# Optimization experiments

Measured on AMD Instinct MI355X. Metric: run time of the kernel, lower is better.

The kernel has to match this reference:

```python
import jax, jax.numpy as jnp
import numpy as np


def _antideriv_tanh(t):
    # int tanh dx = |x| + log1p(exp(-2|x|))  (numerically stable)
    a = jnp.abs(t)
    return a + jnp.log1p(jnp.exp(-2.0 * a))


def _deriv_tanh(t):
    th = jnp.tanh(t)
    return 1.0 - th * th


def setup_inputs() -> dict:
    key = jax.random.key(0)
    ks = jax.random.split(key, 9)
    d, m, nTh, r, nex = 63, 256, 3, 10, 4096
    x = jax.random.normal(ks[0], (nex, d + 1), dtype=jnp.float32)
    W0 = jax.random.normal(ks[1], (m, d + 1), dtype=jnp.float32) / jnp.sqrt(float(d + 1))
    b0 = jax.random.normal(ks[2], (m,), dtype=jnp.float32) * 0.1
    Wd = jax.random.normal(ks[3], (nTh - 1, m, m), dtype=jnp.float32) / jnp.sqrt(float(m))
    bd = jax.random.normal(ks[4], (nTh - 1, m), dtype=jnp.float32) * 0.1
    wv = jax.random.normal(ks[5], (m,), dtype=jnp.float32)
    A = jax.random.normal(ks[6], (r, d + 1), dtype=jnp.float32) / jnp.sqrt(float(d + 1))
    cw = jax.random.normal(ks[7], (d + 1,), dtype=jnp.float32) * 0.1
    cb = jax.random.normal(ks[8], (), dtype=jnp.float32) * 0.1
    return {"x": x, "W0": W0, "b0": b0, "Wd": Wd, "bd": bd, "wv": wv, "A": A, "cw": cw, "cb": cb}


def reference(x, W0, b0, Wd, bd, wv, A, cw, cb):
    """Phi.trHess: returns (grad of Phi wrt x, trace of Hessian of Phi), shapes [nex, d+1], [nex]."""
    nTh = Wd.shape[0] + 1
    h = 1.0 / (nTh - 1)
    m = W0.shape[0]
    nex = x.shape[0]
    d = x.shape[1] - 1

    symA = A.T @ A                                  # [d+1, d+1]

    # ---- forward propagation of ResNN, keeping hidden states u and preactivations ----
    opening = x @ W0.T + b0                         # [nex, m]
    u = [_antideriv_tanh(opening)]
    pre = []                                        # preactivations of layers 1..nTh-1
    feat = u[0]
    for i in range(1, nTh):
        p = feat @ Wd[i - 1].T + bd[i - 1]          # [nex, m]
        pre.append(p)
        feat = feat + h * _antideriv_tanh(p)
        u.append(feat)

    tanhopen = jnp.tanh(opening)                    # [nex, m]

    # ---- backward z chain (Eq. 11): gradient of w'N(x) wrt x ----
    z = [None] * nTh
    for i in range(nTh - 1, 0, -1):
        term = wv[:, None] if i == nTh - 1 else z[i + 1]      # [m,1] or [m,nex]
        z[i] = term + h * (Wd[i - 1].T @ (jnp.tanh(pre[i - 1]).T * term))
    z0 = W0.T @ (tanhopen.T * z[1])                 # [d+1, nex]
    grad = z0 + symA @ x.T + cw[:, None]            # [d+1, nex]

    # ---- trace of Hessian (Eq. 13) ----
    Kopen = W0[:, :d]                               # [m, d]  (spatial part of opening weight)
    temp = _deriv_tanh(opening.T) * z[1]            # [m, nex]
    # sum_{m,d} temp[m,n] * Kopen[m,d]^2
    trH = jnp.einsum('mn,m->n', temp, jnp.sum(Kopen * Kopen, axis=1))

    Jac = Kopen[:, :, None] * tanhopen.T[:, None, :]          # [m, d, nex]
    for i in range(1, nTh):
        KJ = (Wd[i - 1] @ Jac.reshape(m, d * nex)).reshape(m, d, nex)
        term = wv[:, None] if i == nTh - 1 else z[i + 1]
        p = pre[i - 1].T                             # [m, nex]
        t_i = jnp.einsum('mn,mdn->n', _deriv_tanh(p) * term, KJ * KJ)
        trH = trH + h * t_i
        Jac = Jac + h * jnp.tanh(p)[:, None, :] * KJ

    trH = trH + jnp.trace(symA[:d, :d])
    return grad.T, trH
```

## Files before the change

kernel.cpp:

```cpp
#include <hip/hip_runtime.h>
#include <hip/hip_bf16.h>

#define NEX 4096
#define M   256
#define NM  (NEX*M)

typedef __attribute__((ext_vector_type(8))) short short8;
typedef __attribute__((ext_vector_type(16))) float floatx16;
typedef __attribute__((ext_vector_type(4))) unsigned short ushort4v;

__device__ inline unsigned short f2bfu(float x) {
    __hip_bfloat16 h = __float2bfloat16(x);
    union { __hip_bfloat16 b; unsigned short u; } cv; cv.b = h;
    return cv.u;
}
__device__ inline float bfu2f(unsigned short u) {
    union { unsigned short u; __hip_bfloat16 b; } cv; cv.u = u;
    return __bfloat162float(cv.b);
}

__global__ void k_prep(const float* __restrict__ Wd, const float* __restrict__ W0,
                       const float* __restrict__ A,
                       unsigned short* __restrict__ FB,
                       unsigned short* __restrict__ FBT,
                       unsigned short* __restrict__ FW0,
                       unsigned short* __restrict__ FWT,
                       unsigned short* __restrict__ FSA,
                       float* __restrict__ FA,
                       float* __restrict__ ksq, float* __restrict__ trace) {
    int b = blockIdx.x, t = threadIdx.x;
    int lane = t & 63, l31 = lane & 31, lhi = lane >> 5;
    if (b < 64) {
        int combo = b*4 + (t >> 6);
        int l = combo >> 7, rest = combo & 127;
        int mtile = rest >> 4, kstep = rest & 15;
        const float* src = Wd + l*65536 + (mtile*32 + l31)*256 + kstep*16 + lhi*8;
        int off = l*65536 + (mtile*16 + kstep)*512 + lane*8;
        #pragma unroll
        for (int e = 0; e < 8; ++e) FB[off+e] = f2bfu(src[e]);
    } else if (b < 128) {
        int combo = (b-64)*4 + (t >> 6);
        int l = combo >> 7, rest = combo & 127;
        int kt = rest >> 4, ms = rest & 15;
        const float* src = Wd + l*65536 + (ms*16 + lhi*8)*256 + kt*32 + l31;
        int off = l*65536 + (kt*16 + ms)*512 + lane*8;
        #pragma unroll
        for (int e = 0; e < 8; ++e) FBT[off+e] = f2bfu(src[e*256]);
    } else if (b < 136) {
        int combo = (b-128)*4 + (t >> 6);
        int mt = combo >> 2, ks = combo & 3;
        const float* src = W0 + (mt*32 + l31)*64 + ks*16 + lhi*8;
        int off = combo*512 + lane*8;
        #pragma unroll
        for (int e = 0; e < 8; ++e) FW0[off+e] = f2bfu(src[e]);
    } else if (b < 144) {
        int combo = (b-136)*4 + (t >> 6);
        int ct = combo >> 4, ms = combo & 15;
        const float* src = W0 + (ms*16 + lhi*8)*64 + ct*32 + l31;
        int off = combo*512 + lane*8;
        #pragma unroll
        for (int e = 0; e < 8; ++e) FWT[off+e] = f2bfu(src[e*64]);
    } else if (b < 146) {
        int combo = (b-144)*4 + (t >> 6);
        int ct = combo >> 2, ks = combo & 3;
        int c = ct*32 + l31;
        int off = combo*512 + lane*8;
        #pragma unroll
        for (int e = 0; e < 8; ++e) {
            int j = ks*16 + lhi*8 + e;
            float s = 0.f;
            #pragma unroll
            for (int r = 0; r < 10; ++r) s += A[r*64+c] * A[r*64+j];
            FSA[off+e] = f2bfu(s);
        }
    } else if (b == 146) {
        float s = 0.f;
        for (int dd = 0; dd < 63; dd++) { float v = W0[t*64+dd]; s += v*v; }
        ksq[t] = s;
        float p = 0.f;
        for (int idx = t; idx < 630; idx += 256) {
            int r = idx / 63, i = idx % 63;
            float v = A[r*64+i]; p += v*v;
        }
        for (int off = 32; off; off >>= 1) p += __shfl_down(p, off, 64);
        __shared__ float red[4];
        if ((t & 63) == 0) red[t >> 6] = p;
        __syncthreads();
        if (t == 0) trace[0] = red[0]+red[1]+red[2]+red[3];
    } else {
        int q = (b-147)*256 + t;
        int tl = q & 63, frag = q >> 6;
        int d  = (frag >> 4)*32 + (tl & 31);
        int m0 = (frag & 15)*16 + (tl >> 5)*8;
        float* dst = FA + q*8;
        #pragma unroll
        for (int e = 0; e < 8; ++e)
            dst[e] = (d == 63) ? 0.f : W0[(m0 + e)*64 + d];
    }
}

__global__ __launch_bounds__(512, 2) void k_fb(
        const float* __restrict__ x, const float* __restrict__ b0,
        const float* __restrict__ bd, const float* __restrict__ wv,
        const float* __restrict__ cw,
        const unsigned short* __restrict__ FW0,
        const unsigned short* __restrict__ FB,
        const unsigned short* __restrict__ FBT,
        const unsigned short* __restrict__ FWT,
        const unsigned short* __restrict__ FSA,
        float* __restrict__ tanhopen, float* __restrict__ tp0g,
        float* __restrict__ tp1g, float* __restrict__ z2T, float* __restrict__ z1T,
        float* __restrict__ out) {
    __shared__ __align__(16) unsigned short Buh[8192], Bul[8192];
    __shared__ __align__(16) unsigned short Bxh[2048], Bxl[2048];
    __shared__ __align__(16) float bounce[8224];
    __shared__ float b0s[256], bd0s[256], bd1s[256], wvs[256], cws[64];
    int n0 = blockIdx.x * 32, t = threadIdx.x;
    int lane = t & 63, w = t >> 6, l31 = lane & 31, lhi = lane >> 5;

    if (t < 256) { b0s[t]=b0[t]; bd0s[t]=bd[t]; bd1s[t]=bd[256+t]; wvs[t]=wv[t]; }
    if (t < 64) cws[t] = cw[t];
    if (t < 256) {
        int tl = t & 63;
        int ex = tl & 31, k0 = (t >> 6)*16 + (tl >> 5)*8;
        const float* xp = x + (n0+ex)*64 + k0;
        short8 h8, l8;
        #pragma unroll
        for (int e = 0; e < 8; ++e) {
            float v = xp[e];
            unsigned short h = f2bfu(v);
            h8[e] = (short)h; l8[e] = (short)f2bfu(v - bfu2f(h));
        }
        *reinterpret_cast<short8*>(&Bxh[t*8]) = h8;
        *reinterpret_cast<short8*>(&Bxl[t*8]) = l8;
    }
    __syncthreads();

#define MROW(r) (w*32 + ((r)&3) + 8*((r)>>2) + 4*lhi)

#define MFMA2(AH, BH, BL) do { \
    acc = __builtin_amdgcn_mfma_f32_32x32x16_bf16(AH, BH, acc, 0, 0, 0); \
    acc = __builtin_amdgcn_mfma_f32_32x32x16_bf16(AH, BL, acc, 0, 0, 0); \
} while (0)

#define GEMM256(PH) do { \
    for (int ks = 0; ks < 16; ++ks) { \
        short8 Ah = *reinterpret_cast<const short8*>(PH + (w*16+ks)*512 + lane*8); \
        short8 Bh = *reinterpret_cast<const short8*>(&Buh[(ks*64+lane)*8]); \
        short8 Bl = *reinterpret_cast<const short8*>(&Bul[(ks*64+lane)*8]); \
        MFMA2(Ah, Bh, Bl); \
    } \
} while (0)

#define EPILOGUE(SVAL, DST, BVAL) do { \
    __syncthreads(); \
    _Pragma("unroll") \
    for (int r = 0; r < 16; ++r) bounce[l31*257 + MROW(r)] = SVAL[r]; \
    _Pragma("unroll") \
    for (int g = 0; g < 4; ++g) { \
        int ks_ = w*2 + (g>>1); \
        int lp_ = (g&1)*32 + l31; \
        int base_ = (ks_*64 + lp_)*8 + 4*lhi; \
        ushort4v h4, l4; \
        _Pragma("unroll") \
        for (int q = 0; q < 4; ++q) { \
            float v_ = BVAL[g*4+q]; \
            unsigned short h_ = f2bfu(v_); \
            h4[q] = h_; l4[q] = f2bfu(v_ - bfu2f(h_)); \
        } \
        *reinterpret_cast<ushort4v*>(&Buh[base_]) = h4; \
        *reinterpret_cast<ushort4v*>(&Bul[base_]) = l4; \
    } \
    __syncthreads(); \
    _Pragma("unroll") \
    for (int i = 0; i < 16; ++i) { \
        int f = t + i*512; int ex_ = f >> 8, m_ = f & 255; \
        DST[(n0+ex_)*256 + m_] = bounce[ex_*257 + m_]; \
    } \
} while (0)

    floatx16 acc;
    float sv[16], u0v[16], tp0v[16], z2v[16], cf[16];

    #pragma unroll
    for (int r = 0; r < 16; ++r) acc[r] = 0.f;
    #pragma unroll
    for (int ks = 0; ks < 4; ++ks) {
        short8 Ah = *reinterpret_cast<const short8*>(FW0 + (w*4+ks)*512 + lane*8);
        short8 Bh = *reinterpret_cast<const short8*>(&Bxh[(ks*64+lane)*8]);
        short8 Bl = *reinterpret_cast<const short8*>(&Bxl[(ks*64+lane)*8]);
        MFMA2(Ah, Bh, Bl);
    }
    #pragma unroll
    for (int r = 0; r < 16; ++r) {
        float p = acc[r] + b0s[MROW(r)];
        float a = fabsf(p);
        float e = __expf(-2.f*a);
        float th = (1.f - e) * __builtin_amdgcn_rcpf(1.f + e);
        sv[r] = __builtin_copysignf(th, p);
        u0v[r] = a + __logf(1.f + e);
    }
    EPILOGUE(sv, tanhopen, u0v);

    #pragma unroll
    for (int r = 0; r < 16; ++r) acc[r] = 0.f;
    GEMM256(FB);
    #pragma unroll
    for (int r = 0; r < 16; ++r) {
        float p = acc[r] + bd0s[MROW(r)];
        float a = fabsf(p);
        float e = __expf(-2.f*a);
        float th = (1.f - e) * __builtin_amdgcn_rcpf(1.f + e);
        tp0v[r] = __builtin_copysignf(th, p);
        u0v[r] += 0.5f*(a + __logf(1.f + e));
    }
    EPILOGUE(tp0v, tp0g, u0v);

    #pragma unroll
    for (int r = 0; r < 16; ++r) acc[r] = 0.f;
    GEMM256(FB + 65536);
    #pragma unroll
    for (int r = 0; r < 16; ++r) {
        float p = acc[r] + bd1s[MROW(r)];
        float a = fabsf(p);
        float e = __expf(-2.f*a);
        float th = (1.f - e) * __builtin_amdgcn_rcpf(1.f + e);
        cf[r] = __builtin_copysignf(th, p);
        z2v[r] = cf[r] * wvs[MROW(r)];
    }
    EPILOGUE(cf, tp1g, z2v);

    #pragma unroll
    for (int r = 0; r < 16; ++r) acc[r] = 0.f;
    GEMM256(FBT + 65536);
    #pragma unroll
    for (int r = 0; r < 16; ++r) {
        z2v[r] = wvs[MROW(r)] + 0.5f*acc[r];
        cf[r] = tp0v[r] * z2v[r];
    }
    EPILOGUE(z2v, z2T, cf);

    #pragma unroll
    for (int r = 0; r < 16; ++r) acc[r] = 0.f;
    GEMM256(FBT);
    #pragma unroll
    for (int r = 0; r < 16; ++r) {
        z2v[r] += 0.5f*acc[r];
        cf[r] = sv[r] * z2v[r];
    }
    EPILOGUE(z2v, z1T, cf);

    {
        int ct = w >> 2, seg = w & 3;
        #pragma unroll
        for (int r = 0; r < 16; ++r) acc[r] = 0.f;
        #pragma unroll
        for (int k2 = 0; k2 < 4; ++k2) {
            int ms = seg*4 + k2;
            short8 Ah = *reinterpret_cast<const short8*>(FWT + (ct*16+ms)*512 + lane*8);
            short8 Bh = *reinterpret_cast<const short8*>(&Buh[(ms*64+lane)*8]);
            short8 Bl = *reinterpret_cast<const short8*>(&Bul[(ms*64+lane)*8]);
            MFMA2(Ah, Bh, Bl);
        }
        if (seg == 0) {
            #pragma unroll
            for (int ks = 0; ks < 4; ++ks) {
                short8 Ah = *reinterpret_cast<const short8*>(FSA + (ct*4+ks)*512 + lane*8);
                short8 Bh = *reinterpret_cast<const short8*>(&Bxh[(ks*64+lane)*8]);
                short8 Bl = *reinterpret_cast<const short8*>(&Bxl[(ks*64+lane)*8]);
                MFMA2(Ah, Bh, Bl);
            }
        }
        __syncthreads();
        float* gpart = bounce;
        #pragma unroll
        for (int r = 0; r < 16; ++r) gpart[w*1024 + (2*r+lhi)*32 + l31] = acc[r];
        __syncthreads();
        int o0 = t*4, ex = o0 >> 6, c0 = o0 & 63;
        float4 gv;
        #pragma unroll
        for (int jj = 0; jj < 4; ++jj) {
            int c = c0 + jj;
            int ctx = c >> 5, cr = c & 31;
            int lh = (cr >> 2) & 1;
            int rr = (cr & 3) | ((cr >> 3) << 2);
            float s = cws[c];
            #pragma unroll
            for (int sg = 0; sg < 4; ++sg)
                s += gpart[(ctx*4+sg)*1024 + (2*rr+lh)*32 + ex];
            gv[jj] = s;
        }
        *reinterpret_cast<float4*>(&out[(n0+ex)*64 + c0]) = gv;
    }
#undef MROW
#undef MFMA2
#undef GEMM256
#undef EPILOGUE
}

__global__ __launch_bounds__(256, 3) void k_heavy_mfma(
        const float* __restrict__ tanhopen, const float* __restrict__ tp0,
        const float* __restrict__ tp1, const float* __restrict__ z2T,
        const float* __restrict__ z1T, const float* __restrict__ wv,
        const float* __restrict__ FA, const unsigned short* __restrict__ FB,
        const float* __restrict__ ksq, const float* __restrict__ trace,
        float* __restrict__ outTrH) {
    __shared__ __align__(16) unsigned short Bf[16384];
    __shared__ float ss[256], tp0s[256], w1s[256], w2s[256];
    __shared__ float red[4];
    int n = blockIdx.x, t = threadIdx.x;
    int lane = t & 63, w = t >> 6, l31 = lane & 31, lhi = lane >> 5;

    float sv = tanhopen[n*256 + t];
    float a0 = tp0[n*256 + t];
    float a1 = tp1[n*256 + t];
    ss[t] = sv;
    tp0s[t] = a0;
    w1s[t] = (1.f - a0*a0) * z2T[n*256 + t];
    w2s[t] = (1.f - a1*a1) * wv[t];
    float tot = (1.f - sv*sv) * z1T[n*256 + t] * ksq[t];
    __syncthreads();

    #pragma unroll
    for (int i = 0; i < 8; ++i) {
        int q = t + i*256;
        int frag = q >> 6, tl = q & 63;
        int k0 = (frag & 15)*16 + (tl >> 5)*8;
        const float* fp = FA + q*8;
        short8 v8;
        #pragma unroll
        for (int e = 0; e < 8; ++e)
            v8[e] = (short)f2bfu(fp[e] * ss[k0 + e]);
        *reinterpret_cast<short8*>(&Bf[q*8]) = v8;
    }
    __syncthreads();

    floatx16 acc[2][2];
    int mt0 = w*2, mt1 = w*2 + 1;
    float wtot = 0.f;

    const unsigned short* pA0 = FB + mt0*16*512 + lane*8;
    const unsigned short* pA1 = FB + mt1*16*512 + lane*8;
    const unsigned short* qB0 = &Bf[lane*8];
    const unsigned short* qB1 = &Bf[(16*64 + lane)*8];

#define LD8(P, KS) (*reinterpret_cast<const short8*>((P) + (KS)*512))
#define MFMA4(A0_, A1_, B0_, B1_) do { \
    acc[0][0] = __builtin_amdgcn_mfma_f32_32x32x16_bf16(A0_, B0_, acc[0][0], 0, 0, 0); \
    acc[0][1] = __builtin_amdgcn_mfma_f32_32x32x16_bf16(A0_, B1_, acc[0][1], 0, 0, 0); \
    acc[1][0] = __builtin_amdgcn_mfma_f32_32x32x16_bf16(A1_, B0_, acc[1][0], 0, 0, 0); \
    acc[1][1] = __builtin_amdgcn_mfma_f32_32x32x16_bf16(A1_, B1_, acc[1][1], 0, 0, 0); \
} while (0)

    #pragma unroll
    for (int jm = 0; jm < 2; ++jm)
        #pragma unroll
        for (int dh = 0; dh < 2; ++dh)
            #pragma unroll
            for (int r = 0; r < 16; ++r) acc[jm][dh][r] = 0.f;

    {
        short8 A0s[4], A1s[4], B0s[2], B1s[2];
        A0s[0] = LD8(pA0, 0); A1s[0] = LD8(pA1, 0);
        A0s[1] = LD8(pA0, 1); A1s[1] = LD8(pA1, 1);
        A0s[2] = LD8(pA0, 2); A1s[2] = LD8(pA1, 2);
        B0s[0] = LD8(qB0, 0); B1s[0] = LD8(qB1, 0);
        #pragma unroll
        for (int ks = 0; ks < 16; ++ks) {
            if (ks + 3 < 16) {
                A0s[(ks+3)&3] = LD8(pA0, ks+3);
                A1s[(ks+3)&3] = LD8(pA1, ks+3);
            }
            if (ks + 1 < 16) {
                B0s[(ks+1)&1] = LD8(qB0, ks+1);
                B1s[(ks+1)&1] = LD8(qB1, ks+1);
            }
            MFMA4(A0s[ks&3], A1s[ks&3], B0s[ks&1], B1s[ks&1]);
        }
    }

    const unsigned short* pC0 = FB + 65536 + mt0*16*512 + lane*8;
    const unsigned short* pC1 = FB + 65536 + mt1*16*512 + lane*8;
    short8 nA00 = LD8(pC0, 0), nA10 = LD8(pC1, 0);
    short8 nA01 = LD8(pC0, 1), nA11 = LD8(pC1, 1);
    short8 nA02 = LD8(pC0, 2), nA12 = LD8(pC1, 2);

    __syncthreads();

    #pragma unroll
    for (int jm = 0; jm < 2; ++jm) {
        int mt = w*2 + jm;
        #pragma unroll
        for (int g = 0; g < 4; ++g) {
            float w1m[4], tm[4];
            #pragma unroll
            for (int q = 0; q < 4; ++q) {
                int m = mt*32 + 8*g + q + 4*lhi;
                w1m[q] = 0.5f * w1s[m];
                tm[q]  = 0.5f * tp0s[m];
            }
            #pragma unroll
            for (int dh = 0; dh < 2; ++dh) {
                int base = ((dh*16 + mt*2 + (g >> 1))*64
                            + ((g & 1)*32 + l31))*8 + 4*lhi;
                ushort4v old = *reinterpret_cast<ushort4v*>(&Bf[base]);
                ushort4v nw;
                #pragma unroll
                for (int q = 0; q < 4; ++q) {
                    float v = acc[jm][dh][4*g + q];
                    wtot += w1m[q] * v * v;
                    nw[q] = f2bfu(bfu2f(old[q]) + tm[q] * v);
                }
                *reinterpret_cast<ushort4v*>(&Bf[base]) = nw;
            }
        }
    }
    __syncthreads();

    #pragma unroll
    for (int jm = 0; jm < 2; ++jm)
        #pragma unroll
        for (int dh = 0; dh < 2; ++dh)
            #pragma unroll
            for (int r = 0; r < 16; ++r) acc[jm][dh][r] = 0.f;

    {
        short8 A0s[4], A1s[4], B0s[2], B1s[2];
        A0s[0] = nA00; A1s[0] = nA10;
        A0s[1] = nA01; A1s[1] = nA11;
        A0s[2] = nA02; A1s[2] = nA12;
        B0s[0] = LD8(qB0, 0); B1s[0] = LD8(qB1, 0);
        #pragma unroll
        for (int ks = 0; ks < 16; ++ks) {
            if (ks + 3 < 16) {
                A0s[(ks+3)&3] = LD8(pC0, ks+3);
                A1s[(ks+3)&3] = LD8(pC1, ks+3);
            }
            if (ks + 1 < 16) {
                B0s[(ks+1)&1] = LD8(qB0, ks+1);
                B1s[(ks+1)&1] = LD8(qB1, ks+1);
            }
            MFMA4(A0s[ks&3], A1s[ks&3], B0s[ks&1], B1s[ks&1]);
        }
    }
#undef MFMA4
#undef LD8

    #pragma unroll
    for (int jm = 0; jm < 2; ++jm)
        #pragma unroll
        for (int g = 0; g < 4; ++g)
            #pragma unroll
            for (int q = 0; q < 4; ++q) {
                int m = (w*2 + jm)*32 + 8*g + q + 4*lhi;
                float w2m = 0.5f * w2s[m];
                float v0 = acc[jm][0][4*g + q], v1 = acc[jm][1][4*g + q];
                wtot += w2m * (v0*v0 + v1*v1);
            }

    tot += wtot;

    for (int off = 32; off; off >>= 1) tot += __shfl_down(tot, off, 64);
    if (lane == 0) red[w] = tot;
    __syncthreads();
    if (t == 0) outTrH[n] = red[0] + red[1] + red[2] + red[3] + trace[0];
}


extern "C" void kernel_launch(void* const* d_in, const int* in_sizes, int n_in,
                              void* d_out, int out_size, void* d_ws, size_t ws_size,
                              hipStream_t stream) {
    const float* x   = (const float*)d_in[0];
    const float* W0  = (const float*)d_in[1];
    const float* b0  = (const float*)d_in[2];
    const float* Wd  = (const float*)d_in[3];
    const float* bd  = (const float*)d_in[4];
    const float* wv  = (const float*)d_in[5];
    const float* A   = (const float*)d_in[6];
    const float* cw  = (const float*)d_in[7];
    float* out = (float*)d_out;
    float* ws  = (float*)d_ws;

    float* tanhopen = ws;
    float* tp0  = tanhopen + NM;
    float* tp1  = tp0 + NM;
    float* z2T  = tp1 + NM;
    float* z1T  = z2T + NM;
    float* FA   = z1T + NM;
    float* ksq  = FA + 16384;
    float* trace= ksq + 256;
    unsigned short* FB  = (unsigned short*)(trace + 4);
    unsigned short* FBT = FB + 131072;
    unsigned short* FW0 = FBT + 131072;
    unsigned short* FWT = FW0 + 16384;
    unsigned short* FSA = FWT + 16384;

    k_prep<<<155, 256, 0, stream>>>(Wd, W0, A, FB, FBT, FW0, FWT, FSA,
                                    FA, ksq, trace);
    k_fb<<<NEX/32, 512, 0, stream>>>(x, b0, bd, wv, cw,
                                     FW0, FB, FBT, FWT, FSA,
                                     tanhopen, tp0, tp1, z2T, z1T, out);
    k_heavy_mfma<<<NEX, 256, 0, stream>>>(tanhopen, tp0, tp1, z2T, z1T, wv,
                                          FA, FB, ksq, trace, out + NEX*64);
}
```

Before: 117.8 us.

## Switch forward/backward kernel to 16x16x32 MFMA with 16-example tiles

The forward/backward chain kernel now processes 16 examples per 256-thread block instead of 32 per 512-thread block, and uses 16x16x32 bf16 MFMA with four accumulators per wave. It also drops the split-K gradient reduction. The prep kernel gains new fragment layouts for these tiles, while the 32x32 layout is kept for the heavy kernel. Doubling the grid and halving LDS per block is meant to raise parallelism across CUs. In exchange, each weight fragment is reloaded from global/L2 memory twice as often per example.

```diff
diff --git a/kernel.cpp b/kernel.cpp
--- a/kernel.cpp
+++ b/kernel.cpp
@@ -6,6 +6,7 @@
 #define NM  (NEX*M)
 
 typedef __attribute__((ext_vector_type(8))) short short8;
+typedef __attribute__((ext_vector_type(4))) float floatx4;
 typedef __attribute__((ext_vector_type(16))) float floatx16;
 typedef __attribute__((ext_vector_type(4))) unsigned short ushort4v;
 
@@ -21,15 +22,17 @@
 
 __global__ void k_prep(const float* __restrict__ Wd, const float* __restrict__ W0,
                        const float* __restrict__ A,
-                       unsigned short* __restrict__ FB,
-                       unsigned short* __restrict__ FBT,
-                       unsigned short* __restrict__ FW0,
-                       unsigned short* __restrict__ FWT,
-                       unsigned short* __restrict__ FSA,
+                       unsigned short* __restrict__ FB32,
+                       unsigned short* __restrict__ FB16,
+                       unsigned short* __restrict__ FBT16,
+                       unsigned short* __restrict__ FW016,
+                       unsigned short* __restrict__ FWT16,
+                       unsigned short* __restrict__ FSA16,
                        float* __restrict__ FA,
                        float* __restrict__ ksq, float* __restrict__ trace) {
     int b = blockIdx.x, t = threadIdx.x;
     int lane = t & 63, l31 = lane & 31, lhi = lane >> 5;
+    int l15 = lane & 15, lg4 = lane >> 4;
     if (b < 64) {
         int combo = b*4 + (t >> 6);
         int l = combo >> 7, rest = combo & 127;
@@ -37,43 +40,51 @@
         const float* src = Wd + l*65536 + (mtile*32 + l31)*256 + kstep*16 + lhi*8;
         int off = l*65536 + (mtile*16 + kstep)*512 + lane*8;
         #pragma unroll
-        for (int e = 0; e < 8; ++e) FB[off+e] = f2bfu(src[e]);
+        for (int e = 0; e < 8; ++e) FB32[off+e] = f2bfu(src[e]);
     } else if (b < 128) {
         int combo = (b-64)*4 + (t >> 6);
         int l = combo >> 7, rest = combo & 127;
-        int kt = rest >> 4, ms = rest & 15;
-        const float* src = Wd + l*65536 + (ms*16 + lhi*8)*256 + kt*32 + l31;
-        int off = l*65536 + (kt*16 + ms)*512 + lane*8;
-        #pragma unroll
-        for (int e = 0; e < 8; ++e) FBT[off+e] = f2bfu(src[e*256]);
-    } else if (b < 136) {
+        int mt = rest >> 3, ks = rest & 7;
+        const float* src = Wd + l*65536 + (mt*16 + l15)*256 + ks*32 + lg4*8;
+        int off = l*65536 + (mt*8 + ks)*512 + lane*8;
+        #pragma unroll
+        for (int e = 0; e < 8; ++e) FB16[off+e] = f2bfu(src[e]);
+    } else if (b < 192) {
         int combo = (b-128)*4 + (t >> 6);
-        int mt = combo >> 2, ks = combo & 3;
-        const float* src = W0 + (mt*32 + l31)*64 + ks*16 + lhi*8;
+        int l = combo >> 7, rest = combo & 127;
+        int kt = rest >> 3, ms = rest & 7;
+        const float* src = Wd + l*65536 + (ms*32 + lg4*8)*256 + kt*16 + l15;
+        int off = l*65536 + (kt*8 + ms)*512 + lane*8;
+        #pragma unroll
+        for (int e = 0; e < 8; ++e) FBT16[off+e] = f2bfu(src[e*256]);
+    } else if (b < 200) {
+        int combo = (b-192)*4 + (t >> 6);
+        int mt = combo >> 1, ks = combo & 1;
+        const float* src = W0 + (mt*16 + l15)*64 + ks*32 + lg4*8;
         int off = combo*512 + lane*8;
         #pragma unroll
-        for (int e = 0; e < 8; ++e) FW0[off+e] = f2bfu(src[e]);
-    } else if (b < 144) {
-        int combo = (b-136)*4 + (t >> 6);
-        int ct = combo >> 4, ms = combo & 15;
-        const float* src = W0 + (ms*16 + lhi*8)*64 + ct*32 + l31;
+        for (int e = 0; e < 8; ++e) FW016[off+e] = f2bfu(src[e]);
+    } else if (b < 208) {
+        int combo = (b-200)*4 + (t >> 6);
+        int ct = combo >> 3, ms = combo & 7;
+        const float* src = W0 + (ms*32 + lg4*8)*64 + ct*16 + l15;
         int off = combo*512 + lane*8;
         #pragma unroll
-        for (int e = 0; e < 8; ++e) FWT[off+e] = f2bfu(src[e*64]);
-    } else if (b < 146) {
-        int combo = (b-144)*4 + (t >> 6);
-        int ct = combo >> 2, ks = combo & 3;
-        int c = ct*32 + l31;
+        for (int e = 0; e < 8; ++e) FWT16[off+e] = f2bfu(src[e*64]);
+    } else if (b < 210) {
+        int combo = (b-208)*4 + (t >> 6);
+        int ct = combo >> 1, ks = combo & 1;
+        int c = ct*16 + l15;
         int off = combo*512 + lane*8;
         #pragma unroll
         for (int e = 0; e < 8; ++e) {
-            int j = ks*16 + lhi*8 + e;
+            int j = ks*32 + lg4*8 + e;
             float s = 0.f;
             #pragma unroll
             for (int r = 0; r < 10; ++r) s += A[r*64+c] * A[r*64+j];
-            FSA[off+e] = f2bfu(s);
-        }
-    } else if (b == 146) {
+            FSA16[off+e] = f2bfu(s);
+        }
+    } else if (b == 210) {
         float s = 0.f;
         for (int dd = 0; dd < 63; dd++) { float v = W0[t*64+dd]; s += v*v; }
         ksq[t] = s;
@@ -88,7 +99,7 @@
         __syncthreads();
         if (t == 0) trace[0] = red[0]+red[1]+red[2]+red[3];
     } else {
-        int q = (b-147)*256 + t;
+        int q = (b-211)*256 + t;
         int tl = q & 63, frag = q >> 6;
         int d  = (frag >> 4)*32 + (tl & 31);
         int m0 = (frag & 15)*16 + (tl >> 5)*8;
@@ -99,30 +110,30 @@
     }
 }
 
-__global__ __launch_bounds__(512, 2) void k_fb(
+__global__ __launch_bounds__(256, 1) void k_fb(
         const float* __restrict__ x, const float* __restrict__ b0,
         const float* __restrict__ bd, const float* __restrict__ wv,
         const float* __restrict__ cw,
-        const unsigned short* __restrict__ FW0,
-        const unsigned short* __restrict__ FB,
-        const unsigned short* __restrict__ FBT,
-        const unsigned short* __restrict__ FWT,
-        const unsigned short* __restrict__ FSA,
+        const unsigned short* __restrict__ FW016,
+        const unsigned short* __restrict__ FB16,
+        const unsigned short* __restrict__ FBT16,
+        const unsigned short* __restrict__ FWT16,
+        const unsigned short* __restrict__ FSA16,
         float* __restrict__ tanhopen, float* __restrict__ tp0g,
         float* __restrict__ tp1g, float* __restrict__ z2T, float* __restrict__ z1T,
         float* __restrict__ out) {
-    __shared__ __align__(16) unsigned short Buh[8192], Bul[8192];
-    __shared__ __align__(16) unsigned short Bxh[2048], Bxl[2048];
-    __shared__ __align__(16) float bounce[8224];
+    __shared__ __align__(16) unsigned short Buh[4096], Bul[4096];
+    __shared__ __align__(16) unsigned short Bxh[1024], Bxl[1024];
+    __shared__ __align__(16) float bounce[16*257];
     __shared__ float b0s[256], bd0s[256], bd1s[256], wvs[256], cws[64];
-    int n0 = blockIdx.x * 32, t = threadIdx.x;
-    int lane = t & 63, w = t >> 6, l31 = lane & 31, lhi = lane >> 5;
-
-    if (t < 256) { b0s[t]=b0[t]; bd0s[t]=bd[t]; bd1s[t]=bd[256+t]; wvs[t]=wv[t]; }
+    int n0 = blockIdx.x * 16, t = threadIdx.x;
+    int lane = t & 63, w = t >> 6, l15 = lane & 15, lg4 = lane >> 4;
+
+    b0s[t]=b0[t]; bd0s[t]=bd[t]; bd1s[t]=bd[256+t]; wvs[t]=wv[t];
     if (t < 64) cws[t] = cw[t];
-    if (t < 256) {
+    if (t < 128) {
         int tl = t & 63;
-        int ex = tl & 31, k0 = (t >> 6)*16 + (tl >> 5)*8;
+        int ex = tl & 15, k0 = (t >> 6)*32 + (tl >> 4)*8;
         const float* xp = x + (n0+ex)*64 + k0;
         short8 h8, l8;
         #pragma unroll
@@ -136,35 +147,34 @@
     }
     __syncthreads();
 
-#define MROW(r) (w*32 + ((r)&3) + 8*((r)>>2) + 4*lhi)
-
-#define MFMA2(AH, BH, BL) do { \
-    acc = __builtin_amdgcn_mfma_f32_32x32x16_bf16(AH, BH, acc, 0, 0, 0); \
-    acc = __builtin_amdgcn_mfma_f32_32x32x16_bf16(AH, BL, acc, 0, 0, 0); \
-} while (0)
-
-#define GEMM256(PH) do { \
-    for (int ks = 0; ks < 16; ++ks) { \
-        short8 Ah = *reinterpret_cast<const short8*>(PH + (w*16+ks)*512 + lane*8); \
+#define MROW(J, R) ((w*4+(J))*16 + lg4*4 + (R))
+
+#define GEMM256_16(PH) do { \
+    _Pragma("unroll") \
+    for (int ks = 0; ks < 8; ++ks) { \
         short8 Bh = *reinterpret_cast<const short8*>(&Buh[(ks*64+lane)*8]); \
         short8 Bl = *reinterpret_cast<const short8*>(&Bul[(ks*64+lane)*8]); \
-        MFMA2(Ah, Bh, Bl); \
+        _Pragma("unroll") \
+        for (int j = 0; j < 4; ++j) { \
+            short8 Aj = *reinterpret_cast<const short8*>(PH + ((w*4+j)*8 + ks)*512 + lane*8); \
+            acc[j] = __builtin_amdgcn_mfma_f32_16x16x32_bf16(Aj, Bh, acc[j], 0, 0, 0); \
+            acc[j] = __builtin_amdgcn_mfma_f32_16x16x32_bf16(Aj, Bl, acc[j], 0, 0, 0); \
+        } \
     } \
 } while (0)
 
 #define EPILOGUE(SVAL, DST, BVAL) do { \
     __syncthreads(); \
     _Pragma("unroll") \
-    for (int r = 0; r < 16; ++r) bounce[l31*257 + MROW(r)] = SVAL[r]; \
+    for (int v = 0; v < 16; ++v) bounce[l15*257 + MROW(v>>2, v&3)] = SVAL[v]; \
     _Pragma("unroll") \
-    for (int g = 0; g < 4; ++g) { \
-        int ks_ = w*2 + (g>>1); \
-        int lp_ = (g&1)*32 + l31; \
-        int base_ = (ks_*64 + lp_)*8 + 4*lhi; \
+    for (int j = 0; j < 4; ++j) { \
+        int m0_ = (w*4+j)*16 + lg4*4; \
+        int base_ = (((m0_>>5)*64) + ((m0_>>3)&3)*16 + l15)*8 + (m0_&7); \
         ushort4v h4, l4; \
         _Pragma("unroll") \
         for (int q = 0; q < 4; ++q) { \
-            float v_ = BVAL[g*4+q]; \
+            float v_ = BVAL[j*4+q]; \
             unsigned short h_ = f2bfu(v_); \
             h4[q] = h_; l4[q] = f2bfu(v_ - bfu2f(h_)); \
         } \
@@ -174,127 +184,120 @@
     __syncthreads(); \
     _Pragma("unroll") \
     for (int i = 0; i < 16; ++i) { \
-        int f = t + i*512; int ex_ = f >> 8, m_ = f & 255; \
+        int f = t + i*256; int ex_ = f >> 8, m_ = f & 255; \
         DST[(n0+ex_)*256 + m_] = bounce[ex_*257 + m_]; \
     } \
 } while (0)
 
-    floatx16 acc;
+    floatx4 acc[4];
     float sv[16], u0v[16], tp0v[16], z2v[16], cf[16];
 
     #pragma unroll
-    for (int r = 0; r < 16; ++r) acc[r] = 0.f;
-    #pragma unroll
-    for (int ks = 0; ks < 4; ++ks) {
-        short8 Ah = *reinterpret_cast<const short8*>(FW0 + (w*4+ks)*512 + lane*8);
+    for (int j = 0; j < 4; ++j) acc[j] = (floatx4){0.f,0.f,0.f,0.f};
+    #pragma unroll
+    for (int ks = 0; ks < 2; ++ks) {
         short8 Bh = *reinterpret_cast<const short8*>(&Bxh[(ks*64+lane)*8]);
         short8 Bl = *reinterpret_cast<const short8*>(&Bxl[(ks*64+lane)*8]);
-        MFMA2(Ah, Bh, Bl);
-    }
-    #pragma unroll
-    for (int r = 0; r < 16; ++r) {
-        float p = acc[r] + b0s[MROW(r)];
+        #pragma unroll
+        for (int j = 0; j < 4; ++j) {
+            short8 Aj = *reinterpret_cast<const short8*>(FW016 + ((w*4+j)*2 + ks)*512 + lane*8);
+            acc[j] = __builtin_amdgcn_mfma_f32_16x16x32_bf16(Aj, Bh, acc[j], 0, 0, 0);
+            acc[j] = __builtin_amdgcn_mfma_f32_16x16x32_bf16(Aj, Bl, acc[j], 0, 0, 0);
+        }
+    }
+    #pragma unroll
+    for (int v = 0; v < 16; ++v) {
+        float p = acc[v>>2][v&3] + b0s[MROW(v>>2, v&3)];
         float a = fabsf(p);
         float e = __expf(-2.f*a);
         float th = (1.f - e) * __builtin_amdgcn_rcpf(1.f + e);
-        sv[r] = __builtin_copysignf(th, p);
-        u0v[r] = a + __logf(1.f + e);
+        sv[v] = __builtin_copysignf(th, p);
+        u0v[v] = a + __logf(1.f + e);
     }
     EPILOGUE(sv, tanhopen, u0v);
 
     #pragma unroll
-    for (int r = 0; r < 16; ++r) acc[r] = 0.f;
-    GEMM256(FB);
-    #pragma unroll
-    for (int r = 0; r < 16; ++r) {
-        float p = acc[r] + bd0s[MROW(r)];
+    for (int j = 0; j < 4; ++j) acc[j] = (floatx4){0.f,0.f,0.f,0.f};
+    GEMM256_16(FB16);
+    #pragma unroll
+    for (int v = 0; v < 16; ++v) {
+        float p = acc[v>>2][v&3] + bd0s[MROW(v>>2, v&3)];
         float a = fabsf(p);
         float e = __expf(-2.f*a);
         float th = (1.f - e) * __builtin_amdgcn_rcpf(1.f + e);
-        tp0v[r] = __builtin_copysignf(th, p);
-        u0v[r] += 0.5f*(a + __logf(1.f + e));
+        tp0v[v] = __builtin_copysignf(th, p);
+        u0v[v] += 0.5f*(a + __logf(1.f + e));
     }
     EPILOGUE(tp0v, tp0g, u0v);
 
     #pragma unroll
-    for (int r = 0; r < 16; ++r) acc[r] = 0.f;
-    GEMM256(FB + 65536);
-    #pragma unroll
-    for (int r = 0; r < 16; ++r) {
-        float p = acc[r] + bd1s[MROW(r)];
+    for (int j = 0; j < 4; ++j) acc[j] = (floatx4){0.f,0.f,0.f,0.f};
+    GEMM256_16(FB16 + 65536);
+    #pragma unroll
+    for (int v = 0; v < 16; ++v) {
+        float p = acc[v>>2][v&3] + bd1s[MROW(v>>2, v&3)];
         float a = fabsf(p);
         float e = __expf(-2.f*a);
         float th = (1.f - e) * __builtin_amdgcn_rcpf(1.f + e);
-        cf[r] = __builtin_copysignf(th, p);
-        z2v[r] = cf[r] * wvs[MROW(r)];
+        cf[v] = __builtin_copysignf(th, p);
+        z2v[v] = cf[v] * wvs[MROW(v>>2, v&3)];
     }
     EPILOGUE(cf, tp1g, z2v);
 
     #pragma unroll
-    for (int r = 0; r < 16; ++r) acc[r] = 0.f;
-    GEMM256(FBT + 65536);
-    #pragma unroll
-    for (int r = 0; r < 16; ++r) {
-        z2v[r] = wvs[MROW(r)] + 0.5f*acc[r];
-        cf[r] = tp0v[r] * z2v[r];
+    for (int j = 0; j < 4; ++j) acc[j] = (floatx4){0.f,0.f,0.f,0.f};
+    GEMM256_16(FBT16 + 65536);
+    #pragma unroll
+    for (int v = 0; v < 16; ++v) {
+        z2v[v] = wvs[MROW(v>>2, v&3)] + 0.5f*acc[v>>2][v&3];
+        cf[v] = tp0v[v] * z2v[v];
     }
     EPILOGUE(z2v, z2T, cf);
 
     #pragma unroll
-    for (int r = 0; r < 16; ++r) acc[r] = 0.f;
-    GEMM256(FBT);
-    #pragma unroll
-    for (int r = 0; r < 16; ++r) {
-        z2v[r] += 0.5f*acc[r];
-        cf[r] = sv[r] * z2v[r];
+    for (int j = 0; j < 4; ++j) acc[j] = (floatx4){0.f,0.f,0.f,0.f};
+    GEMM256_16(FBT16);
+    #pragma unroll
+    for (int v = 0; v < 16; ++v) {
+        z2v[v] += 0.5f*acc[v>>2][v&3];
+        cf[v] = sv[v] * z2v[v];
     }
     EPILOGUE(z2v, z1T, cf);
 
     {
-        int ct = w >> 2, seg = w & 3;
-        #pragma unroll
-        for (int r = 0; r < 16; ++r) acc[r] = 0.f;
-        #pragma unroll
-        for (int k2 = 0; k2 < 4; ++k2) {
-            int ms = seg*4 + k2;
-            short8 Ah = *reinterpret_cast<const short8*>(FWT + (ct*16+ms)*512 + lane*8);
+        floatx4 ga = (floatx4){0.f,0.f,0.f,0.f};
+        #pragma unroll
+        for (int ms = 0; ms < 8; ++ms) {
             short8 Bh = *reinterpret_cast<const short8*>(&Buh[(ms*64+lane)*8]);
             short8 Bl = *reinterpret_cast<const short8*>(&Bul[(ms*64+lane)*8]);
-            MFMA2(Ah, Bh, Bl);
-        }
-        if (seg == 0) {
-            #pragma unroll
-            for (int ks = 0; ks < 4; ++ks) {
-                short8 Ah = *reinterpret_cast<const short8*>(FSA + (ct*4+ks)*512 + lane*8);
-                short8 Bh = *reinterpret_cast<const short8*>(&Bxh[(ks*64+lane)*8]);
-                short8 Bl = *reinterpret_cast<const short8*>(&Bxl[(ks*64+lane)*8]);
-                MFMA2(Ah, Bh, Bl);
-            }
+            short8 Aj = *reinterpret_cast<const short8*>(FWT16 + (w*8 + ms)*512 + lane*8);
+            ga = __builtin_amdgcn_mfma_f32_16x16x32_bf16(Aj, Bh, ga, 0, 0, 0);
+            ga = __builtin_amdgcn_mfma_f32_16x16x32_bf16(Aj, Bl, ga, 0, 0, 0);
+        }
+        #pragma unroll
+        for (int ks = 0; ks < 2; ++ks) {
+            short8 Bh = *reinterpret_cast<const short8*>(&Bxh[(ks*64+lane)*8]);
+            short8 Bl = *reinterpret_cast<const short8*>(&Bxl[(ks*64+lane)*8]);
+            short8 Aj = *reinterpret_cast<const short8*>(FSA16 + (w*2 + ks)*512 + lane*8);
+            ga = __builtin_amdgcn_mfma_f32_16x16x32_bf16(Aj, Bh, ga, 0, 0, 0);
+            ga = __builtin_amdgcn_mfma_f32_16x16x32_bf16(Aj, Bl, ga, 0, 0, 0);
         }
         __syncthreads();
         float* gpart = bounce;
         #pragma unroll
-        for (int r = 0; r < 16; ++r) gpart[w*1024 + (2*r+lhi)*32 + l31] = acc[r];
+        for (int r = 0; r < 4; ++r) gpart[w*256 + (lg4*4 + r)*16 + l15] = ga[r];
         __syncthreads();
         int o0 = t*4, ex = o0 >> 6, c0 = o0 & 63;
         float4 gv;
         #pragma unroll
         for (int jj = 0; jj < 4; ++jj) {
             int c = c0 + jj;
-            int ctx = c >> 5, cr = c & 31;
-            int lh = (cr >> 2) & 1;
-            int rr = (cr & 3) | ((cr >> 3) << 2);
-            float s = cws[c];
-            #pragma unroll
-            for (int sg = 0; sg < 4; ++sg)
-                s += gpart[(ctx*4+sg)*1024 + (2*rr+lh)*32 + ex];
-            gv[jj] = s;
+            gv[jj] = cws[c] + gpart[(c >> 4)*256 + (c & 15)*16 + ex];
         }
         *reinterpret_cast<float4*>(&out[(n0+ex)*64 + c0]) = gv;
     }
 #undef MROW
-#undef MFMA2
-#undef GEMM256
+#undef GEMM256_16
 #undef EPILOGUE
 }
 
@@ -489,17 +492,18 @@
     float* FA   = z1T + NM;
     float* ksq  = FA + 16384;
     float* trace= ksq + 256;
-    unsigned short* FB  = (unsigned short*)(trace + 4);
-    unsigned short* FBT = FB + 131072;
-    unsigned short* FW0 = FBT + 131072;
-    unsigned short* FWT = FW0 + 16384;
-    unsigned short* FSA = FWT + 16384;
-
-    k_prep<<<155, 256, 0, stream>>>(Wd, W0, A, FB, FBT, FW0, FWT, FSA,
-                                    FA, ksq, trace);
-    k_fb<<<NEX/32, 512, 0, stream>>>(x, b0, bd, wv, cw,
-                                     FW0, FB, FBT, FWT, FSA,
+    unsigned short* FB32  = (unsigned short*)(trace + 4);
+    unsigned short* FB16  = FB32 + 131072;
+    unsigned short* FBT16 = FB16 + 131072;
+    unsigned short* FW016 = FBT16 + 131072;
+    unsigned short* FWT16 = FW016 + 16384;
+    unsigned short* FSA16 = FWT16 + 16384;
+
+    k_prep<<<219, 256, 0, stream>>>(Wd, W0, A, FB32, FB16, FBT16,
+                                    FW016, FWT16, FSA16, FA, ksq, trace);
+    k_fb<<<NEX/16, 256, 0, stream>>>(x, b0, bd, wv, cw,
+                                     FW016, FB16, FBT16, FWT16, FSA16,
                                      tanhopen, tp0, tp1, z2T, z1T, out);
     k_heavy_mfma<<<NEX, 256, 0, stream>>>(tanhopen, tp0, tp1, z2T, z1T, wv,
-                                          FA, FB, ksq, trace, out + NEX*64);
+                                          FA, FB32, ksq, trace, out + NEX*64);
 }
```

Measured after the change: 109.6 us. 6.9% less time.
